# Performance work log

Measured on AMD Instinct MI355X. Metric: run time of the kernel, lower is better.

The kernel has to match this reference:

```python
import jax, jax.numpy as jnp
import numpy as np

K = 3
PAD = 1
EPS = 1e-5


def _unfold(x, k, pad):
    # torch.nn.Unfold(k, dilation=1, padding=pad, stride=1): output [B, C*k*k, L]
    # with channel-major ordering (c, ki, kj) in the second dim.
    B, C, H, W = x.shape
    xp = jnp.pad(x, ((0, 0), (0, 0), (pad, pad), (pad, pad)))
    Ho = H + 2 * pad - k + 1
    Wo = W + 2 * pad - k + 1
    patches = jnp.stack(
        [xp[:, :, i:i + Ho, j:j + Wo] for i in range(k) for j in range(k)],
        axis=2,
    )  # [B, C, k*k, Ho, Wo]
    return patches.reshape(B, C * k * k, Ho * Wo)


def _conv1x1(x, w, b):
    return jnp.einsum('bchw,oc->bohw', x, w) + b[None, :, None, None]


def _bn(x, g, b):
    # training-mode BatchNorm2d: batch stats over (B,H,W), biased variance
    mu = x.mean(axis=(0, 2, 3), keepdims=True)
    var = x.var(axis=(0, 2, 3), keepdims=True)
    return (x - mu) * jax.lax.rsqrt(var + EPS) * g[None, :, None, None] + b[None, :, None, None]


def _tri(x, w, b, g, be):
    return jax.nn.relu(_bn(_conv1x1(x, w, b), g, be))


def reference(x, w1, b1, g1, be1, w2, b2, g2, be2, wf, bf, gf, bef):
    B, C, H, W = x.shape
    k2 = K * K
    c = k2 // 2
    tri1 = _tri(x, w1, b1, g1, be1)  # key map  [B,C,H,W] (m=1)
    tri2 = _tri(x, w2, b2, g2, be2)  # query map
    # NOTE: faithful to source: plain row-major reshape of [B, C*k2, L] -> [B, C, L, k2]
    ku = _unfold(tri1, K, PAD).reshape(B, C, -1, k2)
    qu = _unfold(tri2, K, PAD).reshape(B, C, -1, k2)
    logits = ku * qu[..., c:c + 1] + ku[..., c:c + 1] * qu
    dl_weight = jax.nn.softmax(logits, axis=-1)[:, None]  # [B,1,C,L,k2]
    xu = _unfold(x, K, PAD).reshape(B, 1, C, -1, k2)       # m=1 -> [B,1,C,L,k2]
    # NOTE: faithful to source: row-major reshape to [B, C, k2, L], sum over axis -2
    pre = (dl_weight * xu).reshape(B, C, k2, -1).sum(axis=-2).reshape(B, C, H, W)
    return jax.nn.relu(_bn(_conv1x1(pre, wf, bf), gf, bef))


def setup_inputs() -> dict:
    key = jax.random.key(0)
    B, C, O, H, W = 4, 256, 256, 64, 64
    ks = jax.random.split(key, 4)
    s = 1.0 / np.sqrt(C)
    return {
        'x': jax.random.normal(ks[0], (B, C, H, W), dtype=jnp.float32),
        'w1': jax.random.normal(ks[1], (C, C), dtype=jnp.float32) * s,
        'b1': jnp.zeros((C,), jnp.float32),
        'g1': jnp.ones((C,), jnp.float32),
        'be1': jnp.zeros((C,), jnp.float32),
        'w2': jax.random.normal(ks[2], (C, C), dtype=jnp.float32) * s,
        'b2': jnp.zeros((C,), jnp.float32),
        'g2': jnp.ones((C,), jnp.float32),
        'be2': jnp.zeros((C,), jnp.float32),
        'wf': jax.random.normal(ks[3], (O, C), dtype=jnp.float32) * s,
        'bf': jnp.zeros((O,), jnp.float32),
        'gf': jnp.ones((O,), jnp.float32),
        'bef': jnp.zeros((O,), jnp.float32),
    }
```

## Files before the change

kernel.cpp:

```cpp
#include <hip/hip_runtime.h>

#define L 4096
#define CCH 256
#define NB 4
#define KP 40

typedef __attribute__((ext_vector_type(8))) short short8;
typedef __attribute__((ext_vector_type(4))) float f32x4;

__device__ __forceinline__ unsigned short f2bf(float f) {
    unsigned u = __builtin_bit_cast(unsigned, f);
    u += 0x7FFF + ((u >> 16) & 1);
    return (unsigned short)(u >> 16);
}
__device__ __forceinline__ float bflo(unsigned w) {
    return __builtin_bit_cast(float, w << 16);
}
__device__ __forceinline__ float bfhi(unsigned w) {
    return __builtin_bit_cast(float, w & 0xFFFF0000u);
}

__global__ __launch_bounds__(256, 2) void dual_gemm_k(
    const float* __restrict__ x,
    const float* __restrict__ w1, const float* __restrict__ b1,
    const float* __restrict__ w2, const float* __restrict__ b2,
    float* __restrict__ y1, float* __restrict__ y2)
{
    __shared__ short sA1[128 * KP];
    __shared__ short sA2[128 * KP];
    __shared__ short sB [64 * KP];

    const int tid = threadIdx.x;
    const int l0 = blockIdx.x * 64;
    const int o0 = blockIdx.y * 128;
    const int b  = blockIdx.z;

    const int wv = tid >> 6;
    const int lane = tid & 63;
    const int m = lane & 15;
    const int quad = lane >> 4;

    const float* xb = x + (size_t)b * CCH * L;

    const int sl = tid & 63, soct = tid >> 6;
    const int sr = tid & 127, sh = tid >> 7;

    f32x4 acc1[2][4], acc2[2][4];
    #pragma unroll
    for (int io = 0; io < 2; ++io)
        #pragma unroll
        for (int jl = 0; jl < 4; ++jl) {
            acc1[io][jl] = (f32x4){0.f,0.f,0.f,0.f};
            acc2[io][jl] = (f32x4){0.f,0.f,0.f,0.f};
        }

    for (int s = 0; s < 8; ++s) {
        const int k0 = s * 32;
        __syncthreads();
        {
            const float* xs = xb + (size_t)(k0 + soct * 8) * L + l0 + sl;
            short8 v;
            #pragma unroll
            for (int j = 0; j < 8; ++j) v[j] = (short)f2bf(xs[(size_t)j * L]);
            *(short8*)&sB[sl * KP + soct * 8] = v;
        }
        {
            const float4* wp = (const float4*)&w1[(size_t)(o0 + sr) * CCH + k0 + sh * 16];
            float4 c0 = wp[0], c1 = wp[1], c2 = wp[2], c3 = wp[3];
            short8 p0 = {(short)f2bf(c0.x),(short)f2bf(c0.y),(short)f2bf(c0.z),(short)f2bf(c0.w),
                         (short)f2bf(c1.x),(short)f2bf(c1.y),(short)f2bf(c1.z),(short)f2bf(c1.w)};
            short8 p1 = {(short)f2bf(c2.x),(short)f2bf(c2.y),(short)f2bf(c2.z),(short)f2bf(c2.w),
                         (short)f2bf(c3.x),(short)f2bf(c3.y),(short)f2bf(c3.z),(short)f2bf(c3.w)};
            *(short8*)&sA1[sr * KP + sh * 16]     = p0;
            *(short8*)&sA1[sr * KP + sh * 16 + 8] = p1;
            const float4* wq = (const float4*)&w2[(size_t)(o0 + sr) * CCH + k0 + sh * 16];
            float4 d0 = wq[0], d1 = wq[1], d2 = wq[2], d3 = wq[3];
            short8 q0 = {(short)f2bf(d0.x),(short)f2bf(d0.y),(short)f2bf(d0.z),(short)f2bf(d0.w),
                         (short)f2bf(d1.x),(short)f2bf(d1.y),(short)f2bf(d1.z),(short)f2bf(d1.w)};
            short8 q1 = {(short)f2bf(d2.x),(short)f2bf(d2.y),(short)f2bf(d2.z),(short)f2bf(d2.w),
                         (short)f2bf(d3.x),(short)f2bf(d3.y),(short)f2bf(d3.z),(short)f2bf(d3.w)};
            *(short8*)&sA2[sr * KP + sh * 16]     = q0;
            *(short8*)&sA2[sr * KP + sh * 16 + 8] = q1;
        }
        __syncthreads();
        short8 a1[2], a2[2], bf[4];
        #pragma unroll
        for (int io = 0; io < 2; ++io) {
            a1[io] = *(const short8*)&sA1[(wv * 32 + io * 16 + m) * KP + quad * 8];
            a2[io] = *(const short8*)&sA2[(wv * 32 + io * 16 + m) * KP + quad * 8];
        }
        #pragma unroll
        for (int jl = 0; jl < 4; ++jl)
            bf[jl] = *(const short8*)&sB[(jl * 16 + m) * KP + quad * 8];
        #pragma unroll
        for (int io = 0; io < 2; ++io)
            #pragma unroll
            for (int jl = 0; jl < 4; ++jl) {
                acc1[io][jl] = __builtin_amdgcn_mfma_f32_16x16x32_bf16(a1[io], bf[jl], acc1[io][jl], 0, 0, 0);
                acc2[io][jl] = __builtin_amdgcn_mfma_f32_16x16x32_bf16(a2[io], bf[jl], acc2[io][jl], 0, 0, 0);
            }
    }

    #pragma unroll
    for (int io = 0; io < 2; ++io)
        #pragma unroll
        for (int reg = 0; reg < 4; ++reg) {
            const int o = o0 + wv * 32 + io * 16 + quad * 4 + reg;
            const float bb1 = b1[o], bb2 = b2[o];
            const size_t ro = ((size_t)b * CCH + o) * L + l0 + m;
            #pragma unroll
            for (int jl = 0; jl < 4; ++jl) {
                y1[ro + jl * 16] = acc1[io][jl][reg] + bb1;
                y2[ro + jl * 16] = acc2[io][jl][reg] + bb2;
            }
        }
}

__global__ __launch_bounds__(256, 2) void single_gemm_k(
    const float* __restrict__ x,
    const float* __restrict__ w, const float* __restrict__ bb,
    float* __restrict__ y)
{
    __shared__ short sA[128 * KP];
    __shared__ short sB[64 * KP];

    const int tid = threadIdx.x;
    const int l0 = blockIdx.x * 64;
    const int o0 = blockIdx.y * 128;
    const int b  = blockIdx.z;

    const int wv = tid >> 6;
    const int lane = tid & 63;
    const int m = lane & 15;
    const int quad = lane >> 4;

    const float* xb = x + (size_t)b * CCH * L;

    const int sl = tid & 63, soct = tid >> 6;
    const int sr = tid & 127, sh = tid >> 7;

    f32x4 acc[2][4];
    #pragma unroll
    for (int io = 0; io < 2; ++io)
        #pragma unroll
        for (int jl = 0; jl < 4; ++jl)
            acc[io][jl] = (f32x4){0.f,0.f,0.f,0.f};

    for (int s = 0; s < 8; ++s) {
        const int k0 = s * 32;
        __syncthreads();
        {
            const float* xs = xb + (size_t)(k0 + soct * 8) * L + l0 + sl;
            short8 v;
            #pragma unroll
            for (int j = 0; j < 8; ++j) v[j] = (short)f2bf(xs[(size_t)j * L]);
            *(short8*)&sB[sl * KP + soct * 8] = v;
        }
        {
            const float4* wp = (const float4*)&w[(size_t)(o0 + sr) * CCH + k0 + sh * 16];
            float4 c0 = wp[0], c1 = wp[1], c2 = wp[2], c3 = wp[3];
            short8 p0 = {(short)f2bf(c0.x),(short)f2bf(c0.y),(short)f2bf(c0.z),(short)f2bf(c0.w),
                         (short)f2bf(c1.x),(short)f2bf(c1.y),(short)f2bf(c1.z),(short)f2bf(c1.w)};
            short8 p1 = {(short)f2bf(c2.x),(short)f2bf(c2.y),(short)f2bf(c2.z),(short)f2bf(c2.w),
                         (short)f2bf(c3.x),(short)f2bf(c3.y),(short)f2bf(c3.z),(short)f2bf(c3.w)};
            *(short8*)&sA[sr * KP + sh * 16]     = p0;
            *(short8*)&sA[sr * KP + sh * 16 + 8] = p1;
        }
        __syncthreads();
        short8 a[2], bf[4];
        #pragma unroll
        for (int io = 0; io < 2; ++io)
            a[io] = *(const short8*)&sA[(wv * 32 + io * 16 + m) * KP + quad * 8];
        #pragma unroll
        for (int jl = 0; jl < 4; ++jl)
            bf[jl] = *(const short8*)&sB[(jl * 16 + m) * KP + quad * 8];
        #pragma unroll
        for (int io = 0; io < 2; ++io)
            #pragma unroll
            for (int jl = 0; jl < 4; ++jl)
                acc[io][jl] = __builtin_amdgcn_mfma_f32_16x16x32_bf16(a[io], bf[jl], acc[io][jl], 0, 0, 0);
    }

    #pragma unroll
    for (int io = 0; io < 2; ++io)
        #pragma unroll
        for (int reg = 0; reg < 4; ++reg) {
            const int o = o0 + wv * 32 + io * 16 + quad * 4 + reg;
            const float b0 = bb[o];
            const size_t ro = ((size_t)b * CCH + o) * L + l0 + m;
            #pragma unroll
            for (int jl = 0; jl < 4; ++jl)
                y[ro + jl * 16] = acc[io][jl][reg] + b0;
        }
}

__device__ __forceinline__ void bn_stats_body(
    const float* y, const float* gamma, const float* beta,
    float* scale, float* shift, int c, int tid)
{
    float s = 0.f, s2 = 0.f;
    for (int b = 0; b < NB; ++b) {
        const float4* p = (const float4*)(y + ((size_t)b * CCH + c) * L);
        #pragma unroll
        for (int r = 0; r < 4; ++r) {
            float4 v = p[r * 256 + tid];
            s  += v.x + v.y + v.z + v.w;
            s2 += v.x * v.x + v.y * v.y + v.z * v.z + v.w * v.w;
        }
    }
    #pragma unroll
    for (int off = 32; off > 0; off >>= 1) {
        s  += __shfl_down(s, off);
        s2 += __shfl_down(s2, off);
    }
    __shared__ float red[2][4];
    if ((tid & 63) == 0) { red[0][tid >> 6] = s; red[1][tid >> 6] = s2; }
    __syncthreads();
    if (tid == 0) {
        float S  = red[0][0] + red[0][1] + red[0][2] + red[0][3];
        float S2 = red[1][0] + red[1][1] + red[1][2] + red[1][3];
        const float invN = 1.f / (NB * (float)L);
        float mean = S * invN;
        float var  = S2 * invN - mean * mean;
        float rstd = rsqrtf(var + 1e-5f);
        float g = gamma[c];
        scale[c] = g * rstd;
        shift[c] = beta[c] - mean * g * rstd;
    }
}

__global__ __launch_bounds__(256) void bn_stats_k(
    const float* __restrict__ y, const float* __restrict__ gamma,
    const float* __restrict__ beta,
    float* __restrict__ scale, float* __restrict__ shift)
{
    bn_stats_body(y, gamma, beta, scale, shift, blockIdx.x, threadIdx.x);
}

__global__ __launch_bounds__(256) void bn_stats2_k(
    const float* __restrict__ y1, const float* __restrict__ g1, const float* __restrict__ be1,
    float* __restrict__ sc1, float* __restrict__ sh1,
    const float* __restrict__ y2, const float* __restrict__ g2, const float* __restrict__ be2,
    float* __restrict__ sc2, float* __restrict__ sh2)
{
    const int c = blockIdx.x & 255;
    if (blockIdx.x < 256) bn_stats_body(y1, g1, be1, sc1, sh1, c, threadIdx.x);
    else                  bn_stats_body(y2, g2, be2, sc2, sh2, c, threadIdx.x);
}

__global__ __launch_bounds__(512, 4) void attention_k(
    const float* __restrict__ x,
    const float* __restrict__ y1,
    const float* __restrict__ y2,
    const float* __restrict__ s1sc, const float* __restrict__ s1sh,
    const float* __restrict__ s2sc, const float* __restrict__ s2sh,
    float* __restrict__ pre)
{
    __shared__ unsigned sKQ[L];
    __shared__ float    sXv[L];
    __shared__ uint2    sCI[L];

    const int bc = blockIdx.x;
    const int tid = threadIdx.x;
    const int ch = bc & 255;
    const size_t off = (size_t)bc * L;

    const float sc1 = s1sc[ch], sh1 = s1sh[ch];
    const float sc2 = s2sc[ch], sh2 = s2sh[ch];

    const float4* k4 = (const float4*)(y1 + off);
    const float4* q4 = (const float4*)(y2 + off);
    const float4* x4 = (const float4*)(x + off);

    #pragma unroll
    for (int r = 0; r < 2; ++r) {
        int i = r * 512 + tid;
        float4 a = k4[i];
        float4 q = q4[i];
        float kk[4] = {a.x, a.y, a.z, a.w};
        float qq[4] = {q.x, q.y, q.z, q.w};
        #pragma unroll
        for (int u = 0; u < 4; ++u) {
            unsigned pk = f2bf(fmaxf(fmaf(kk[u], sc1, sh1), 0.f));
            unsigned pq = f2bf(fmaxf(fmaf(qq[u], sc2, sh2), 0.f));
            sKQ[i * 4 + u] = pk | (pq << 16);
        }
        ((float4*)sXv)[i] = x4[i];
    }
    __syncthreads();

    #pragma unroll
    for (int r = 0; r < 8; ++r) {
        const int lp = r * 512 + tid;
        const int base = 9 * lp;
        float kv[9], qv[9];
        unsigned cw = 0;
        #pragma unroll
        for (int j = 0; j < 9; ++j) {
            int f = base + j;
            int t = f >> 12;
            int l = f & 4095;
            int di = (t * 86) >> 8;
            int dj = t - di * 3;
            int ii = (l >> 6) + di - 1;
            int jj = (l & 63) + dj - 1;
            bool ok = ((unsigned)ii < 64u) && ((unsigned)jj < 64u);
            int src = ((ii << 6) + jj) & 4095;
            unsigned w = sKQ[src];
            w = ok ? w : 0u;
            if (j == 4) cw = w;
            kv[j] = bflo(w);
            qv[j] = bfhi(w);
        }
        const float kc = kv[4], qc = qv[4];
        float s01 = __expf(kv[0] * qc + kc * qv[0]) + __expf(kv[1] * qc + kc * qv[1]);
        float s23 = __expf(kv[2] * qc + kc * qv[2]) + __expf(kv[3] * qc + kc * qv[3]);
        float s45 = __expf(kv[4] * qc + kc * qv[4]) + __expf(kv[5] * qc + kc * qv[5]);
        float s67 = __expf(kv[6] * qc + kc * qv[6]) + __expf(kv[7] * qc + kc * qv[7]);
        float s = ((s01 + s23) + (s45 + s67)) + __expf(kv[8] * qc + kc * qv[8]);
        uint2 ci;
        ci.x = cw;
        ci.y = __builtin_bit_cast(unsigned, -__logf(s));
        sCI[lp] = ci;
    }
    __syncthreads();

    #pragma unroll
    for (int r = 0; r < 8; ++r) {
        const int l = r * 512 + tid;
        const int li = l >> 6, lj = l & 63;
        float acc = 0.f;
        #pragma unroll
        for (int t = 0; t < 9; ++t) {
            const int f = (t << 12) + l;
            const unsigned lp = (unsigned)f / 9u;
            uint2 ci = sCI[lp];
            const float kc = bflo(ci.x), qc = bfhi(ci.x);
            const float cn = __builtin_bit_cast(float, ci.y);
            const int di = t / 3, dj = t % 3;
            int ii = li + di - 1;
            int jj = lj + dj - 1;
            bool ok = ((unsigned)ii < 64u) && ((unsigned)jj < 64u);
            int src = ((ii << 6) + jj) & 4095;
            unsigned w = sKQ[src];
            float xj = sXv[src];
            w  = ok ? w : 0u;
            xj = ok ? xj : 0.f;
            const float kj = bflo(w), qj = bfhi(w);
            float e = __expf(fmaf(kj, qc, fmaf(kc, qj, cn)));
            acc = fmaf(e, xj, acc);
        }
        pre[off + l] = acc;
    }
}

__global__ __launch_bounds__(256) void bn_apply_k(
    const float* __restrict__ yf,
    const float* __restrict__ scale, const float* __restrict__ shift,
    float* __restrict__ out)
{
    int i = blockIdx.x * 256 + threadIdx.x;
    int o = (i >> 10) & 255;
    float sc = scale[o], sh = shift[o];
    float4 v = ((const float4*)yf)[i];
    v.x = fmaxf(fmaf(v.x, sc, sh), 0.f);
    v.y = fmaxf(fmaf(v.y, sc, sh), 0.f);
    v.z = fmaxf(fmaf(v.z, sc, sh), 0.f);
    v.w = fmaxf(fmaf(v.w, sc, sh), 0.f);
    ((float4*)out)[i] = v;
}

extern "C" void kernel_launch(void* const* d_in, const int* in_sizes, int n_in,
                              void* d_out, int out_size, void* d_ws, size_t ws_size,
                              hipStream_t stream) {
    const float* x   = (const float*)d_in[0];
    const float* w1  = (const float*)d_in[1];
    const float* b1  = (const float*)d_in[2];
    const float* g1  = (const float*)d_in[3];
    const float* be1 = (const float*)d_in[4];
    const float* w2  = (const float*)d_in[5];
    const float* b2  = (const float*)d_in[6];
    const float* g2  = (const float*)d_in[7];
    const float* be2 = (const float*)d_in[8];
    const float* wf  = (const float*)d_in[9];
    const float* bf  = (const float*)d_in[10];
    const float* gf  = (const float*)d_in[11];
    const float* bef = (const float*)d_in[12];
    float* out = (float*)d_out;

    float* ws = (float*)d_ws;
    const size_t NEL = (size_t)NB * CCH * L;
    float* y1 = ws;
    float* y2 = ws + NEL;
    float* st = ws + 2 * NEL;
    float* s1sc = st,        *s1sh = st + 256;
    float* s2sc = st + 512,  *s2sh = st + 768;
    float* sfsc = st + 1024, *sfsh = st + 1280;

    dim3 gg(64, 2, 4);
    dual_gemm_k<<<gg, 256, 0, stream>>>(x, w1, b1, w2, b2, y1, y2);
    bn_stats2_k<<<512, 256, 0, stream>>>(y1, g1, be1, s1sc, s1sh,
                                         y2, g2, be2, s2sc, s2sh);
    attention_k<<<NB * CCH, 512, 0, stream>>>(x, y1, y2, s1sc, s1sh, s2sc, s2sh, y2);
    single_gemm_k<<<gg, 256, 0, stream>>>(y2, wf, bf, y1);
    bn_stats_k<<<256, 256, 0, stream>>>(y1, gf, bef, sfsc, sfsh);
    bn_apply_k<<<4096, 256, 0, stream>>>(y1, sfsc, sfsh, out);
}
```

Measured before the change: 186.4 us.

## Fuse BN statistics into GEMM epilogues via atomics and store intermediates as bf16

Measured after the change: 221.4 us. 1.19x slower.

```diff
diff --git a/kernel.cpp b/kernel.cpp
--- a/kernel.cpp
+++ b/kernel.cpp
@@ -7,6 +7,7 @@
 
 typedef __attribute__((ext_vector_type(8))) short short8;
 typedef __attribute__((ext_vector_type(4))) float f32x4;
+typedef unsigned short ushort_t;
 
 __device__ __forceinline__ unsigned short f2bf(float f) {
     unsigned u = __builtin_bit_cast(unsigned, f);
@@ -24,7 +25,9 @@
     const float* __restrict__ x,
     const float* __restrict__ w1, const float* __restrict__ b1,
     const float* __restrict__ w2, const float* __restrict__ b2,
-    float* __restrict__ y1, float* __restrict__ y2)
+    ushort_t* __restrict__ y1, ushort_t* __restrict__ y2,
+    float* __restrict__ gs1, float* __restrict__ gss1,
+    float* __restrict__ gs2, float* __restrict__ gss2)
 {
     __shared__ short sA1[128 * KP];
     __shared__ short sA2[128 * KP];
@@ -108,18 +111,33 @@
             const int o = o0 + wv * 32 + io * 16 + quad * 4 + reg;
             const float bb1 = b1[o], bb2 = b2[o];
             const size_t ro = ((size_t)b * CCH + o) * L + l0 + m;
+            float s1 = 0.f, q1 = 0.f, s2 = 0.f, q2 = 0.f;
             #pragma unroll
             for (int jl = 0; jl < 4; ++jl) {
-                y1[ro + jl * 16] = acc1[io][jl][reg] + bb1;
-                y2[ro + jl * 16] = acc2[io][jl][reg] + bb2;
+                float v1 = acc1[io][jl][reg] + bb1;
+                float v2 = acc2[io][jl][reg] + bb2;
+                y1[ro + jl * 16] = f2bf(v1);
+                y2[ro + jl * 16] = f2bf(v2);
+                s1 += v1; q1 += v1 * v1;
+                s2 += v2; q2 += v2 * v2;
+            }
+            #pragma unroll
+            for (int d = 1; d < 16; d <<= 1) {
+                s1 += __shfl_xor(s1, d); q1 += __shfl_xor(q1, d);
+                s2 += __shfl_xor(s2, d); q2 += __shfl_xor(q2, d);
+            }
+            if (m == 0) {
+                atomicAdd(&gs1[o], s1); atomicAdd(&gss1[o], q1);
+                atomicAdd(&gs2[o], s2); atomicAdd(&gss2[o], q2);
             }
         }
 }
 
 __global__ __launch_bounds__(256, 2) void single_gemm_k(
-    const float* __restrict__ x,
+    const ushort_t* __restrict__ x,
     const float* __restrict__ w, const float* __restrict__ bb,
-    float* __restrict__ y)
+    ushort_t* __restrict__ y,
+    float* __restrict__ gsf, float* __restrict__ gssf)
 {
     __shared__ short sA[128 * KP];
     __shared__ short sB[64 * KP];
@@ -134,7 +152,7 @@
     const int m = lane & 15;
     const int quad = lane >> 4;
 
-    const float* xb = x + (size_t)b * CCH * L;
+    const ushort_t* xb = x + (size_t)b * CCH * L;
 
     const int sl = tid & 63, soct = tid >> 6;
     const int sr = tid & 127, sh = tid >> 7;
@@ -150,10 +168,10 @@
         const int k0 = s * 32;
         __syncthreads();
         {
-            const float* xs = xb + (size_t)(k0 + soct * 8) * L + l0 + sl;
+            const ushort_t* xs = xb + (size_t)(k0 + soct * 8) * L + l0 + sl;
             short8 v;
             #pragma unroll
-            for (int j = 0; j < 8; ++j) v[j] = (short)f2bf(xs[(size_t)j * L]);
+            for (int j = 0; j < 8; ++j) v[j] = (short)xs[(size_t)j * L];
             *(short8*)&sB[sl * KP + soct * 8] = v;
         }
         {
@@ -188,73 +206,32 @@
             const int o = o0 + wv * 32 + io * 16 + quad * 4 + reg;
             const float b0 = bb[o];
             const size_t ro = ((size_t)b * CCH + o) * L + l0 + m;
-            #pragma unroll
-            for (int jl = 0; jl < 4; ++jl)
-                y[ro + jl * 16] = acc[io][jl][reg] + b0;
-        }
-}
-
-__device__ __forceinline__ void bn_stats_body(
-    const float* y, const float* gamma, const float* beta,
-    float* scale, float* shift, int c, int tid)
-{
-    float s = 0.f, s2 = 0.f;
-    for (int b = 0; b < NB; ++b) {
-        const float4* p = (const float4*)(y + ((size_t)b * CCH + c) * L);
-        #pragma unroll
-        for (int r = 0; r < 4; ++r) {
-            float4 v = p[r * 256 + tid];
-            s  += v.x + v.y + v.z + v.w;
-            s2 += v.x * v.x + v.y * v.y + v.z * v.z + v.w * v.w;
-        }
-    }
-    #pragma unroll
-    for (int off = 32; off > 0; off >>= 1) {
-        s  += __shfl_down(s, off);
-        s2 += __shfl_down(s2, off);
-    }
-    __shared__ float red[2][4];
-    if ((tid & 63) == 0) { red[0][tid >> 6] = s; red[1][tid >> 6] = s2; }
-    __syncthreads();
-    if (tid == 0) {
-        float S  = red[0][0] + red[0][1] + red[0][2] + red[0][3];
-        float S2 = red[1][0] + red[1][1] + red[1][2] + red[1][3];
-        const float invN = 1.f / (NB * (float)L);
-        float mean = S * invN;
-        float var  = S2 * invN - mean * mean;
-        float rstd = rsqrtf(var + 1e-5f);
-        float g = gamma[c];
-        scale[c] = g * rstd;
-        shift[c] = beta[c] - mean * g * rstd;
-    }
-}
-
-__global__ __launch_bounds__(256) void bn_stats_k(
-    const float* __restrict__ y, const float* __restrict__ gamma,
-    const float* __restrict__ beta,
-    float* __restrict__ scale, float* __restrict__ shift)
-{
-    bn_stats_body(y, gamma, beta, scale, shift, blockIdx.x, threadIdx.x);
-}
-
-__global__ __launch_bounds__(256) void bn_stats2_k(
-    const float* __restrict__ y1, const float* __restrict__ g1, const float* __restrict__ be1,
-    float* __restrict__ sc1, float* __restrict__ sh1,
-    const float* __restrict__ y2, const float* __restrict__ g2, const float* __restrict__ be2,
-    float* __restrict__ sc2, float* __restrict__ sh2)
-{
-    const int c = blockIdx.x & 255;
-    if (blockIdx.x < 256) bn_stats_body(y1, g1, be1, sc1, sh1, c, threadIdx.x);
-    else                  bn_stats_body(y2, g2, be2, sc2, sh2, c, threadIdx.x);
+            float s = 0.f, q = 0.f;
+            #pragma unroll
+            for (int jl = 0; jl < 4; ++jl) {
+                float v = acc[io][jl][reg] + b0;
+                y[ro + jl * 16] = f2bf(v);
+                s += v; q += v * v;
+            }
+            #pragma unroll
+            for (int d = 1; d < 16; d <<= 1) {
+                s += __shfl_xor(s, d); q += __shfl_xor(q, d);
+            }
+            if (m == 0) {
+                atomicAdd(&gsf[o], s); atomicAdd(&gssf[o], q);
+            }
+        }
 }
 
 __global__ __launch_bounds__(512, 4) void attention_k(
     const float* __restrict__ x,
-    const float* __restrict__ y1,
-    const float* __restrict__ y2,
-    const float* __restrict__ s1sc, const float* __restrict__ s1sh,
-    const float* __restrict__ s2sc, const float* __restrict__ s2sh,
-    float* __restrict__ pre)
+    const ushort_t* __restrict__ y1,
+    const ushort_t* __restrict__ y2,
+    const float* __restrict__ g1, const float* __restrict__ be1,
+    const float* __restrict__ g2, const float* __restrict__ be2,
+    const float* __restrict__ gs1, const float* __restrict__ gss1,
+    const float* __restrict__ gs2, const float* __restrict__ gss2,
+    ushort_t* __restrict__ pre)
 {
     __shared__ unsigned sKQ[L];
     __shared__ float    sXv[L];
@@ -265,27 +242,34 @@
     const int ch = bc & 255;
     const size_t off = (size_t)bc * L;
 
-    const float sc1 = s1sc[ch], sh1 = s1sh[ch];
-    const float sc2 = s2sc[ch], sh2 = s2sh[ch];
-
-    const float4* k4 = (const float4*)(y1 + off);
-    const float4* q4 = (const float4*)(y2 + off);
+    const float invN = 1.f / (NB * (float)L);
+    float mu1 = gs1[ch] * invN;
+    float va1 = gss1[ch] * invN - mu1 * mu1;
+    float r1 = rsqrtf(va1 + 1e-5f);
+    const float sc1 = g1[ch] * r1, sh1 = be1[ch] - mu1 * g1[ch] * r1;
+    float mu2 = gs2[ch] * invN;
+    float va2 = gss2[ch] * invN - mu2 * mu2;
+    float r2 = rsqrtf(va2 + 1e-5f);
+    const float sc2 = g2[ch] * r2, sh2 = be2[ch] - mu2 * g2[ch] * r2;
+
     const float4* x4 = (const float4*)(x + off);
 
-    #pragma unroll
-    for (int r = 0; r < 2; ++r) {
-        int i = r * 512 + tid;
-        float4 a = k4[i];
-        float4 q = q4[i];
-        float kk[4] = {a.x, a.y, a.z, a.w};
-        float qq[4] = {q.x, q.y, q.z, q.w};
+    {
+        uint4 ak = ((const uint4*)(y1 + off))[tid];
+        uint4 aq = ((const uint4*)(y2 + off))[tid];
+        unsigned wks[4] = {ak.x, ak.y, ak.z, ak.w};
+        unsigned wqs[4] = {aq.x, aq.y, aq.z, aq.w};
         #pragma unroll
         for (int u = 0; u < 4; ++u) {
-            unsigned pk = f2bf(fmaxf(fmaf(kk[u], sc1, sh1), 0.f));
-            unsigned pq = f2bf(fmaxf(fmaf(qq[u], sc2, sh2), 0.f));
-            sKQ[i * 4 + u] = pk | (pq << 16);
-        }
-        ((float4*)sXv)[i] = x4[i];
+            float klo = fmaxf(fmaf(bflo(wks[u]), sc1, sh1), 0.f);
+            float khi = fmaxf(fmaf(bfhi(wks[u]), sc1, sh1), 0.f);
+            float qlo = fmaxf(fmaf(bflo(wqs[u]), sc2, sh2), 0.f);
+            float qhi = fmaxf(fmaf(bfhi(wqs[u]), sc2, sh2), 0.f);
+            sKQ[8 * tid + 2 * u]     = (unsigned)f2bf(klo) | ((unsigned)f2bf(qlo) << 16);
+            sKQ[8 * tid + 2 * u + 1] = (unsigned)f2bf(khi) | ((unsigned)f2bf(qhi) << 16);
+        }
+        ((float4*)sXv)[2 * tid]     = x4[2 * tid];
+        ((float4*)sXv)[2 * tid + 1] = x4[2 * tid + 1];
     }
     __syncthreads();
 
@@ -350,24 +334,37 @@
             float e = __expf(fmaf(kj, qc, fmaf(kc, qj, cn)));
             acc = fmaf(e, xj, acc);
         }
-        pre[off + l] = acc;
+        pre[off + l] = f2bf(acc);
     }
 }
 
 __global__ __launch_bounds__(256) void bn_apply_k(
-    const float* __restrict__ yf,
-    const float* __restrict__ scale, const float* __restrict__ shift,
+    const ushort_t* __restrict__ yf,
+    const float* __restrict__ gf, const float* __restrict__ bef,
+    const float* __restrict__ gsf, const float* __restrict__ gssf,
     float* __restrict__ out)
 {
-    int i = blockIdx.x * 256 + threadIdx.x;
-    int o = (i >> 10) & 255;
-    float sc = scale[o], sh = shift[o];
-    float4 v = ((const float4*)yf)[i];
-    v.x = fmaxf(fmaf(v.x, sc, sh), 0.f);
-    v.y = fmaxf(fmaf(v.y, sc, sh), 0.f);
-    v.z = fmaxf(fmaf(v.z, sc, sh), 0.f);
-    v.w = fmaxf(fmaf(v.w, sc, sh), 0.f);
-    ((float4*)out)[i] = v;
+    const int i = blockIdx.x * 256 + threadIdx.x;
+    const int ch = (i >> 9) & 255;
+    const float invN = 1.f / (NB * (float)L);
+    float mu = gsf[ch] * invN;
+    float va = gssf[ch] * invN - mu * mu;
+    float r = rsqrtf(va + 1e-5f);
+    const float sc = gf[ch] * r, sh = bef[ch] - mu * gf[ch] * r;
+
+    uint4 v = ((const uint4*)yf)[i];
+    unsigned w[4] = {v.x, v.y, v.z, v.w};
+    float4 o0, o1;
+    o0.x = fmaxf(fmaf(bflo(w[0]), sc, sh), 0.f);
+    o0.y = fmaxf(fmaf(bfhi(w[0]), sc, sh), 0.f);
+    o0.z = fmaxf(fmaf(bflo(w[1]), sc, sh), 0.f);
+    o0.w = fmaxf(fmaf(bfhi(w[1]), sc, sh), 0.f);
+    o1.x = fmaxf(fmaf(bflo(w[2]), sc, sh), 0.f);
+    o1.y = fmaxf(fmaf(bfhi(w[2]), sc, sh), 0.f);
+    o1.z = fmaxf(fmaf(bflo(w[3]), sc, sh), 0.f);
+    o1.w = fmaxf(fmaf(bfhi(w[3]), sc, sh), 0.f);
+    ((float4*)out)[2 * i]     = o0;
+    ((float4*)out)[2 * i + 1] = o1;
 }
 
 extern "C" void kernel_launch(void* const* d_in, const int* in_sizes, int n_in,
@@ -388,21 +385,24 @@
     const float* bef = (const float*)d_in[12];
     float* out = (float*)d_out;
 
-    float* ws = (float*)d_ws;
     const size_t NEL = (size_t)NB * CCH * L;
-    float* y1 = ws;
-    float* y2 = ws + NEL;
-    float* st = ws + 2 * NEL;
-    float* s1sc = st,        *s1sh = st + 256;
-    float* s2sc = st + 512,  *s2sh = st + 768;
-    float* sfsc = st + 1024, *sfsh = st + 1280;
+    ushort_t* y1b = (ushort_t*)d_ws;
+    ushort_t* y2b = y1b + NEL;
+    float* st = (float*)(y2b + NEL);
+    float* gs1 = st,        *gss1 = st + 256;
+    float* gs2 = st + 512,  *gss2 = st + 768;
+    float* gsf = st + 1024, *gssf = st + 1280;
+
+    hipMemsetAsync(st, 0, 1536 * sizeof(float), stream);
 
     dim3 gg(64, 2, 4);
-    dual_gemm_k<<<gg, 256, 0, stream>>>(x, w1, b1, w2, b2, y1, y2);
-    bn_stats2_k<<<512, 256, 0, stream>>>(y1, g1, be1, s1sc, s1sh,
-                                         y2, g2, be2, s2sc, s2sh);
-    attention_k<<<NB * CCH, 512, 0, stream>>>(x, y1, y2, s1sc, s1sh, s2sc, s2sh, y2);
-    single_gemm_k<<<gg, 256, 0, stream>>>(y2, wf, bf, y1);
-    bn_stats_k<<<256, 256, 0, stream>>>(y1, gf, bef, sfsc, sfsh);
-    bn_apply_k<<<4096, 256, 0, stream>>>(y1, sfsc, sfsh, out);
-}
+    dual_gemm_k<<<gg, 256, 0, stream>>>(x, w1, b1, w2, b2, y1b, y2b,
+                                        gs1, gss1, gs2, gss2);
+    attention_k<<<NB * CCH, 512, 0, stream>>>(x, y1b, y2b,
+                                              g1, be1, g2, be2,
+                                              gs1, gss1, gs2, gss2,
+                                              y2b);
+    single_gemm_k<<<gg, 256, 0, stream>>>(y2b, wf, bf, y1b,
+                                          gsf, gssf);
+    bn_apply_k<<<(int)(NEL / 2048), 256, 0, stream>>>(y1b, gf, bef, gsf, gssf, out);
+}
```

## Store intermediate activations in bf16 across all pipeline kernels

Applied to the files above, without the earlier changes.

Result: faster. 180.9 us (-3.0%).

```diff
diff --git a/kernel.cpp b/kernel.cpp
--- a/kernel.cpp
+++ b/kernel.cpp
@@ -7,6 +7,7 @@
 
 typedef __attribute__((ext_vector_type(8))) short short8;
 typedef __attribute__((ext_vector_type(4))) float f32x4;
+typedef unsigned short ushort_t;
 
 __device__ __forceinline__ unsigned short f2bf(float f) {
     unsigned u = __builtin_bit_cast(unsigned, f);
@@ -24,7 +25,7 @@
     const float* __restrict__ x,
     const float* __restrict__ w1, const float* __restrict__ b1,
     const float* __restrict__ w2, const float* __restrict__ b2,
-    float* __restrict__ y1, float* __restrict__ y2)
+    ushort_t* __restrict__ y1, ushort_t* __restrict__ y2)
 {
     __shared__ short sA1[128 * KP];
     __shared__ short sA2[128 * KP];
@@ -110,16 +111,16 @@
             const size_t ro = ((size_t)b * CCH + o) * L + l0 + m;
             #pragma unroll
             for (int jl = 0; jl < 4; ++jl) {
-                y1[ro + jl * 16] = acc1[io][jl][reg] + bb1;
-                y2[ro + jl * 16] = acc2[io][jl][reg] + bb2;
+                y1[ro + jl * 16] = f2bf(acc1[io][jl][reg] + bb1);
+                y2[ro + jl * 16] = f2bf(acc2[io][jl][reg] + bb2);
             }
         }
 }
 
 __global__ __launch_bounds__(256, 2) void single_gemm_k(
-    const float* __restrict__ x,
+    const ushort_t* __restrict__ x,
     const float* __restrict__ w, const float* __restrict__ bb,
-    float* __restrict__ y)
+    ushort_t* __restrict__ y)
 {
     __shared__ short sA[128 * KP];
     __shared__ short sB[64 * KP];
@@ -134,7 +135,7 @@
     const int m = lane & 15;
     const int quad = lane >> 4;
 
-    const float* xb = x + (size_t)b * CCH * L;
+    const ushort_t* xb = x + (size_t)b * CCH * L;
 
     const int sl = tid & 63, soct = tid >> 6;
     const int sr = tid & 127, sh = tid >> 7;
@@ -150,10 +151,10 @@
         const int k0 = s * 32;
         __syncthreads();
         {
-            const float* xs = xb + (size_t)(k0 + soct * 8) * L + l0 + sl;
+            const ushort_t* xs = xb + (size_t)(k0 + soct * 8) * L + l0 + sl;
             short8 v;
             #pragma unroll
-            for (int j = 0; j < 8; ++j) v[j] = (short)f2bf(xs[(size_t)j * L]);
+            for (int j = 0; j < 8; ++j) v[j] = (short)xs[(size_t)j * L];
             *(short8*)&sB[sl * KP + soct * 8] = v;
         }
         {
@@ -190,22 +191,27 @@
             const size_t ro = ((size_t)b * CCH + o) * L + l0 + m;
             #pragma unroll
             for (int jl = 0; jl < 4; ++jl)
-                y[ro + jl * 16] = acc[io][jl][reg] + b0;
+                y[ro + jl * 16] = f2bf(acc[io][jl][reg] + b0);
         }
 }
 
 __device__ __forceinline__ void bn_stats_body(
-    const float* y, const float* gamma, const float* beta,
+    const ushort_t* y, const float* gamma, const float* beta,
     float* scale, float* shift, int c, int tid)
 {
     float s = 0.f, s2 = 0.f;
     for (int b = 0; b < NB; ++b) {
-        const float4* p = (const float4*)(y + ((size_t)b * CCH + c) * L);
-        #pragma unroll
-        for (int r = 0; r < 4; ++r) {
-            float4 v = p[r * 256 + tid];
-            s  += v.x + v.y + v.z + v.w;
-            s2 += v.x * v.x + v.y * v.y + v.z * v.z + v.w * v.w;
+        const uint4* p = (const uint4*)(y + ((size_t)b * CCH + c) * L);
+        #pragma unroll
+        for (int r = 0; r < 2; ++r) {
+            uint4 v = p[r * 256 + tid];
+            unsigned w[4] = {v.x, v.y, v.z, v.w};
+            #pragma unroll
+            for (int u = 0; u < 4; ++u) {
+                float a = bflo(w[u]), bb = bfhi(w[u]);
+                s  += a + bb;
+                s2 += a * a + bb * bb;
+            }
         }
     }
     #pragma unroll
@@ -230,7 +236,7 @@
 }
 
 __global__ __launch_bounds__(256) void bn_stats_k(
-    const float* __restrict__ y, const float* __restrict__ gamma,
+    const ushort_t* __restrict__ y, const float* __restrict__ gamma,
     const float* __restrict__ beta,
     float* __restrict__ scale, float* __restrict__ shift)
 {
@@ -238,9 +244,9 @@
 }
 
 __global__ __launch_bounds__(256) void bn_stats2_k(
-    const float* __restrict__ y1, const float* __restrict__ g1, const float* __restrict__ be1,
+    const ushort_t* __restrict__ y1, const float* __restrict__ g1, const float* __restrict__ be1,
     float* __restrict__ sc1, float* __restrict__ sh1,
-    const float* __restrict__ y2, const float* __restrict__ g2, const float* __restrict__ be2,
+    const ushort_t* __restrict__ y2, const float* __restrict__ g2, const float* __restrict__ be2,
     float* __restrict__ sc2, float* __restrict__ sh2)
 {
     const int c = blockIdx.x & 255;
@@ -250,11 +256,11 @@
 
 __global__ __launch_bounds__(512, 4) void attention_k(
     const float* __restrict__ x,
-    const float* __restrict__ y1,
-    const float* __restrict__ y2,
+    const ushort_t* __restrict__ y1,
+    const ushort_t* __restrict__ y2,
     const float* __restrict__ s1sc, const float* __restrict__ s1sh,
     const float* __restrict__ s2sc, const float* __restrict__ s2sh,
-    float* __restrict__ pre)
+    ushort_t* __restrict__ pre)
 {
     __shared__ unsigned sKQ[L];
     __shared__ float    sXv[L];
@@ -268,24 +274,24 @@
     const float sc1 = s1sc[ch], sh1 = s1sh[ch];
     const float sc2 = s2sc[ch], sh2 = s2sh[ch];
 
-    const float4* k4 = (const float4*)(y1 + off);
-    const float4* q4 = (const float4*)(y2 + off);
     const float4* x4 = (const float4*)(x + off);
 
-    #pragma unroll
-    for (int r = 0; r < 2; ++r) {
-        int i = r * 512 + tid;
-        float4 a = k4[i];
-        float4 q = q4[i];
-        float kk[4] = {a.x, a.y, a.z, a.w};
-        float qq[4] = {q.x, q.y, q.z, q.w};
+    {
+        uint4 ak = ((const uint4*)(y1 + off))[tid];
+        uint4 aq = ((const uint4*)(y2 + off))[tid];
+        unsigned wks[4] = {ak.x, ak.y, ak.z, ak.w};
+        unsigned wqs[4] = {aq.x, aq.y, aq.z, aq.w};
         #pragma unroll
         for (int u = 0; u < 4; ++u) {
-            unsigned pk = f2bf(fmaxf(fmaf(kk[u], sc1, sh1), 0.f));
-            unsigned pq = f2bf(fmaxf(fmaf(qq[u], sc2, sh2), 0.f));
-            sKQ[i * 4 + u] = pk | (pq << 16);
-        }
-        ((float4*)sXv)[i] = x4[i];
+            float klo = fmaxf(fmaf(bflo(wks[u]), sc1, sh1), 0.f);
+            float khi = fmaxf(fmaf(bfhi(wks[u]), sc1, sh1), 0.f);
+            float qlo = fmaxf(fmaf(bflo(wqs[u]), sc2, sh2), 0.f);
+            float qhi = fmaxf(fmaf(bfhi(wqs[u]), sc2, sh2), 0.f);
+            sKQ[8 * tid + 2 * u]     = (unsigned)f2bf(klo) | ((unsigned)f2bf(qlo) << 16);
+            sKQ[8 * tid + 2 * u + 1] = (unsigned)f2bf(khi) | ((unsigned)f2bf(qhi) << 16);
+        }
+        ((float4*)sXv)[2 * tid]     = x4[2 * tid];
+        ((float4*)sXv)[2 * tid + 1] = x4[2 * tid + 1];
     }
     __syncthreads();
 
@@ -350,24 +356,32 @@
             float e = __expf(fmaf(kj, qc, fmaf(kc, qj, cn)));
             acc = fmaf(e, xj, acc);
         }
-        pre[off + l] = acc;
+        pre[off + l] = f2bf(acc);
     }
 }
 
 __global__ __launch_bounds__(256) void bn_apply_k(
-    const float* __restrict__ yf,
+    const ushort_t* __restrict__ yf,
     const float* __restrict__ scale, const float* __restrict__ shift,
     float* __restrict__ out)
 {
-    int i = blockIdx.x * 256 + threadIdx.x;
-    int o = (i >> 10) & 255;
-    float sc = scale[o], sh = shift[o];
-    float4 v = ((const float4*)yf)[i];
-    v.x = fmaxf(fmaf(v.x, sc, sh), 0.f);
-    v.y = fmaxf(fmaf(v.y, sc, sh), 0.f);
-    v.z = fmaxf(fmaf(v.z, sc, sh), 0.f);
-    v.w = fmaxf(fmaf(v.w, sc, sh), 0.f);
-    ((float4*)out)[i] = v;
+    const int i = blockIdx.x * 256 + threadIdx.x;
+    const int ch = (i >> 9) & 255;
+    const float sc = scale[ch], sh = shift[ch];
+
+    uint4 v = ((const uint4*)yf)[i];
+    unsigned w[4] = {v.x, v.y, v.z, v.w};
+    float4 o0, o1;
+    o0.x = fmaxf(fmaf(bflo(w[0]), sc, sh), 0.f);
+    o0.y = fmaxf(fmaf(bfhi(w[0]), sc, sh), 0.f);
+    o0.z = fmaxf(fmaf(bflo(w[1]), sc, sh), 0.f);
+    o0.w = fmaxf(fmaf(bfhi(w[1]), sc, sh), 0.f);
+    o1.x = fmaxf(fmaf(bflo(w[2]), sc, sh), 0.f);
+    o1.y = fmaxf(fmaf(bfhi(w[2]), sc, sh), 0.f);
+    o1.z = fmaxf(fmaf(bflo(w[3]), sc, sh), 0.f);
+    o1.w = fmaxf(fmaf(bfhi(w[3]), sc, sh), 0.f);
+    ((float4*)out)[2 * i]     = o0;
+    ((float4*)out)[2 * i + 1] = o1;
 }
 
 extern "C" void kernel_launch(void* const* d_in, const int* in_sizes, int n_in,
@@ -388,21 +402,22 @@
     const float* bef = (const float*)d_in[12];
     float* out = (float*)d_out;
 
-    float* ws = (float*)d_ws;
     const size_t NEL = (size_t)NB * CCH * L;
-    float* y1 = ws;
-    float* y2 = ws + NEL;
-    float* st = ws + 2 * NEL;
+    ushort_t* y1b = (ushort_t*)d_ws;
+    ushort_t* y2b = y1b + NEL;
+    float* st = (float*)(y2b + NEL);
     float* s1sc = st,        *s1sh = st + 256;
     float* s2sc = st + 512,  *s2sh = st + 768;
     float* sfsc = st + 1024, *sfsh = st + 1280;
 
     dim3 gg(64, 2, 4);
-    dual_gemm_k<<<gg, 256, 0, stream>>>(x, w1, b1, w2, b2, y1, y2);
-    bn_stats2_k<<<512, 256, 0, stream>>>(y1, g1, be1, s1sc, s1sh,
-                                         y2, g2, be2, s2sc, s2sh);
-    attention_k<<<NB * CCH, 512, 0, stream>>>(x, y1, y2, s1sc, s1sh, s2sc, s2sh, y2);
-    single_gemm_k<<<gg, 256, 0, stream>>>(y2, wf, bf, y1);
-    bn_stats_k<<<256, 256, 0, stream>>>(y1, gf, bef, sfsc, sfsh);
-    bn_apply_k<<<4096, 256, 0, stream>>>(y1, sfsc, sfsh, out);
-}
+    dual_gemm_k<<<gg, 256, 0, stream>>>(x, w1, b1, w2, b2, y1b, y2b);
+    bn_stats2_k<<<512, 256, 0, stream>>>(y1b, g1, be1, s1sc, s1sh,
+                                         y2b, g2, be2, s2sc, s2sh);
+    attention_k<<<NB * CCH, 512, 0, stream>>>(x, y1b, y2b,
+                                              s1sc, s1sh, s2sc, s2sh,
+                                              y2b);
+    single_gemm_k<<<gg, 256, 0, stream>>>(y2b, wf, bf, y1b);
+    bn_stats_k<<<256, 256, 0, stream>>>(y1b, gf, bef, sfsc, sfsh);
+    bn_apply_k<<<(int)(NEL / 2048), 256, 0, stream>>>(y1b, sfsc, sfsh, out);
+}
```
